# Kernel tuning notes

Hardware: AMD Instinct MI355X
Metric: run time of the kernel (lower is better)

The kernel has to match this reference:

```python
import jax, jax.numpy as jnp
import numpy as np

N_NODES = 50000
N_EDGES = 800000
IN_C = 128
OUT_C = 128


def setup_inputs() -> dict:
    key = jax.random.key(0)
    k1, k2, k3 = jax.random.split(key, 3)
    x = jax.random.normal(k1, (N_NODES, IN_C), dtype=jnp.float32)
    edge_index = jax.random.randint(k2, (2, N_EDGES), 0, N_NODES, dtype=jnp.int64)
    weight = jax.random.normal(k3, (IN_C, OUT_C), dtype=jnp.float32) * 0.01
    bias = jnp.zeros((OUT_C,), dtype=jnp.float32)
    return {"x": x, "edge_index": edge_index, "weight": weight, "bias": bias}


def reference(x, edge_index, weight, bias):
    num_nodes = x.shape[0]
    # add self-loops
    loop = jnp.arange(num_nodes, dtype=edge_index.dtype)
    src = jnp.concatenate([edge_index[0], loop])  # [E + N]
    dst = jnp.concatenate([edge_index[1], loop])  # [E + N]
    # in-degree (incl. self-loops) via scatter-add
    deg = jax.ops.segment_sum(jnp.ones_like(dst, dtype=x.dtype), dst,
                              num_segments=num_nodes)
    # deg >= 1 due to self-loops, but guard inf like the original
    deg_inv_sqrt = jnp.where(deg > 0, jax.lax.rsqrt(deg), 0.0)
    norm = deg_inv_sqrt[src] * deg_inv_sqrt[dst]  # [E + N]
    x_transformed = x @ weight  # [N, out_c]
    messages = x_transformed[src] * norm[:, None]  # [E + N, out_c]
    out = jax.ops.segment_sum(messages, dst, num_segments=num_nodes)
    return out + bias
```

## Files before the change

### kernel.cpp

```cpp
#include <hip/hip_runtime.h>

#define C 128
#define CHUNK 4096

typedef short bf16x8 __attribute__((ext_vector_type(8)));
typedef float f32x4 __attribute__((ext_vector_type(4)));

__device__ inline unsigned short f2bf(float f) {
    unsigned u = __float_as_uint(f);
    u += 0x7fffu + ((u >> 16) & 1u);
    return (unsigned short)(u >> 16);
}

__device__ inline unsigned pk2bf(float lo, float hi) {
    return (unsigned)f2bf(lo) | ((unsigned)f2bf(hi) << 16);
}

__global__ __launch_bounds__(256) void k1_hist(
        const int* __restrict__ ei, int e, int* __restrict__ H,
        int nblocks, int nbuck,
        const float* __restrict__ W, unsigned short* __restrict__ Wt) {
    int b = blockIdx.x;
    int t = threadIdx.x;
    if (b >= nblocks) {
        int i = (b - nblocks) * 256 + t;
        int nn = i >> 7, k = i & 127;
        Wt[nn * 128 + k] = f2bf(W[k * 128 + nn]);
        return;
    }
    __shared__ int h[256];
    h[t] = 0;
    __syncthreads();
    int base = b * CHUNK;
    int lim = min(CHUNK, e - base);
    for (int i = t; i < lim; i += 256)
        atomicAdd(&h[ei[e + base + i] >> 8], 1);
    __syncthreads();
    if (t < nbuck) H[t * nblocks + b] = h[t];
}

__global__ __launch_bounds__(256) void k2a_rowscan(
        int* __restrict__ H, int* __restrict__ tot, int nblocks) {
    __shared__ int s[256];
    int g = blockIdx.x, t = threadIdx.x;
    int v = (t < nblocks) ? H[g * nblocks + t] : 0;
    s[t] = v;
    __syncthreads();
    for (int off = 1; off < 256; off <<= 1) {
        int u = (t >= off) ? s[t - off] : 0;
        __syncthreads();
        s[t] += u;
        __syncthreads();
    }
    if (t < nblocks) H[g * nblocks + t] = s[t] - v;
    if (t == 255) tot[g] = s[255];
}

__global__ __launch_bounds__(256) void k2b_bucketscan(
        const int* __restrict__ tot, int* __restrict__ bbase, int nbuck, int e) {
    __shared__ int s[256];
    int t = threadIdx.x;
    int v = (t < nbuck) ? tot[t] : 0;
    s[t] = v;
    __syncthreads();
    for (int off = 1; off < 256; off <<= 1) {
        int u = (t >= off) ? s[t - off] : 0;
        __syncthreads();
        s[t] += u;
        __syncthreads();
    }
    if (t < nbuck) bbase[t] = s[t] - v;
    if (t == 0) bbase[nbuck] = e;
}

__global__ __launch_bounds__(256) void k3_scatter(
        const int* __restrict__ ei, int e, const int* __restrict__ H,
        const int* __restrict__ bbase,
        unsigned* __restrict__ staging, int nblocks, int nbuck) {
    __shared__ int cur[256];
    int b = blockIdx.x, t = threadIdx.x;
    if (t < nbuck) cur[t] = bbase[t] + H[t * nblocks + b];
    __syncthreads();
    int base = b * CHUNK;
    int lim = min(CHUNK, e - base);
    for (int i = t; i < lim; i += 256) {
        int src = ei[base + i];
        int dst = ei[e + base + i];
        int pos = atomicAdd(&cur[dst >> 8], 1);
        staging[pos] = (unsigned)src | ((unsigned)(dst & 255) << 16);
    }
}

__global__ __launch_bounds__(256) void k4_finalize(
        const unsigned* __restrict__ staging, const int* __restrict__ bbase,
        int* __restrict__ row_ptr, float* __restrict__ dis,
        unsigned short* __restrict__ srcs, int n) {
    __shared__ int sc[256];
    __shared__ int cur[256];
    int g = blockIdx.x, t = threadIdx.x;
    int s0 = bbase[g], s1 = bbase[g + 1];
    sc[t] = 0;
    __syncthreads();
    for (int i = s0 + t; i < s1; i += 256)
        atomicAdd(&sc[staging[i] >> 16], 1);
    __syncthreads();
    int v = sc[t];
    __syncthreads();
    for (int off = 1; off < 256; off <<= 1) {
        int u = (t >= off) ? sc[t - off] : 0;
        __syncthreads();
        sc[t] += u;
        __syncthreads();
    }
    int excl = sc[t] - v;
    int idx = g * 256 + t;
    if (idx <= n) row_ptr[idx] = s0 + excl;
    if (idx < n) dis[idx] = rsqrtf((float)(v + 1));
    cur[t] = s0 + excl;
    __syncthreads();
    for (int i = s0 + t; i < s1; i += 256) {
        unsigned rec = staging[i];
        int pos = atomicAdd(&cur[rec >> 16], 1);
        srcs[pos] = (unsigned short)(rec & 0xffffu);
    }
}

__global__ __launch_bounds__(256) void gemm_mfma(
        const float* __restrict__ x, const unsigned short* __restrict__ Wt,
        const float* __restrict__ dis, unsigned short* __restrict__ xts, int n) {
    const int lane = threadIdx.x & 63;
    const int wave = threadIdx.x >> 6;
    const int m = lane & 15;
    const int q = lane >> 4;
    const int r0 = blockIdx.x * 64 + wave * 16;
    const int row = r0 + m;
    const int rowc = (row < n) ? row : (n - 1);

    f32x4 acc[8];
#pragma unroll
    for (int nt = 0; nt < 8; ++nt) acc[nt] = (f32x4){0.f, 0.f, 0.f, 0.f};

#pragma unroll
    for (int kb = 0; kb < 4; ++kb) {
        const int k0 = kb * 32 + q * 8;
        const float4* xp = (const float4*)(x + (size_t)rowc * 128 + k0);
        float4 xa = xp[0];
        float4 xb = xp[1];
        union { unsigned u[4]; bf16x8 v; } af;
        af.u[0] = pk2bf(xa.x, xa.y);
        af.u[1] = pk2bf(xa.z, xa.w);
        af.u[2] = pk2bf(xb.x, xb.y);
        af.u[3] = pk2bf(xb.z, xb.w);
#pragma unroll
        for (int nt = 0; nt < 8; ++nt) {
            bf16x8 bf = *(const bf16x8*)(Wt + (size_t)(nt * 16 + m) * 128 + k0);
            acc[nt] = __builtin_amdgcn_mfma_f32_16x16x32_bf16(af.v, bf, acc[nt], 0, 0, 0);
        }
    }

    float dv[4];
    int gr[4];
#pragma unroll
    for (int r = 0; r < 4; ++r) {
        gr[r] = r0 + q * 4 + r;
        dv[r] = dis[(gr[r] < n) ? gr[r] : (n - 1)];
    }
#pragma unroll
    for (int nt = 0; nt < 8; ++nt) {
        int col = nt * 16 + m;
#pragma unroll
        for (int r = 0; r < 4; ++r) {
            if (gr[r] < n)
                xts[(size_t)gr[r] * 128 + col] = f2bf(acc[nt][r] * dv[r]);
        }
    }
}

__device__ inline void acc8(float* a, uint4 w) {
    a[0] += __uint_as_float(w.x << 16);
    a[1] += __uint_as_float(w.x & 0xffff0000u);
    a[2] += __uint_as_float(w.y << 16);
    a[3] += __uint_as_float(w.y & 0xffff0000u);
    a[4] += __uint_as_float(w.z << 16);
    a[5] += __uint_as_float(w.z & 0xffff0000u);
    a[6] += __uint_as_float(w.w << 16);
    a[7] += __uint_as_float(w.w & 0xffff0000u);
}

__global__ void gather3(const int* __restrict__ row_ptr,
                        const unsigned short* __restrict__ srcs,
                        const unsigned short* __restrict__ xts,
                        const float* __restrict__ dis,
                        const float* __restrict__ bias, float* __restrict__ out, int n) {
    int node = blockIdx.x * 16 + (threadIdx.x >> 4);
    int q = threadIdx.x & 15;
    if (node >= n) return;
    const uint4* x4 = (const uint4*)xts;
    int start = row_ptr[node];
    int end = row_ptr[node + 1];
    float a0[8] = {0, 0, 0, 0, 0, 0, 0, 0};
    float a1[8] = {0, 0, 0, 0, 0, 0, 0, 0};
    acc8(a0, x4[node * 16 + q]);
    int j = start;
    for (; j + 4 <= end; j += 4) {
        uint4 m0 = x4[(int)srcs[j] * 16 + q];
        uint4 m1 = x4[(int)srcs[j + 1] * 16 + q];
        uint4 m2 = x4[(int)srcs[j + 2] * 16 + q];
        uint4 m3 = x4[(int)srcs[j + 3] * 16 + q];
        acc8(a0, m0);
        acc8(a1, m1);
        acc8(a0, m2);
        acc8(a1, m3);
    }
    for (; j < end; ++j) acc8(a0, x4[(int)srcs[j] * 16 + q]);
    float d = dis[node];
    const float4 b0 = ((const float4*)bias)[q * 2];
    const float4 b1 = ((const float4*)bias)[q * 2 + 1];
    float4 o0, o1;
    o0.x = (a0[0] + a1[0]) * d + b0.x;
    o0.y = (a0[1] + a1[1]) * d + b0.y;
    o0.z = (a0[2] + a1[2]) * d + b0.z;
    o0.w = (a0[3] + a1[3]) * d + b0.w;
    o1.x = (a0[4] + a1[4]) * d + b1.x;
    o1.y = (a0[5] + a1[5]) * d + b1.y;
    o1.z = (a0[6] + a1[6]) * d + b1.z;
    o1.w = (a0[7] + a1[7]) * d + b1.w;
    float4* op = (float4*)(out + node * 128 + q * 8);
    op[0] = o0;
    op[1] = o1;
}

extern "C" void kernel_launch(void* const* d_in, const int* in_sizes, int n_in,
                              void* d_out, int out_size, void* d_ws, size_t ws_size,
                              hipStream_t stream) {
    const float* x    = (const float*)d_in[0];
    const int*   ei   = (const int*)d_in[1];
    const float* W    = (const float*)d_in[2];
    const float* bias = (const float*)d_in[3];
    float* out = (float*)d_out;

    const int n = in_sizes[0] / C;
    const int e = in_sizes[1] / 2;
    const int nblocks = (e + CHUNK - 1) / CHUNK;
    const int nbuck = (n + 255) >> 8;

    char* p = (char*)d_ws;
    auto alloc = [&](size_t bytes) {
        char* r = p;
        p += (bytes + 15) & ~(size_t)15;
        return (void*)r;
    };
    int*      H       = (int*)alloc((size_t)nbuck * nblocks * 4);
    int*      tot     = (int*)alloc(nbuck * 4);
    int*      bbase   = (int*)alloc((nbuck + 1) * 4);
    unsigned* staging = (unsigned*)alloc((size_t)e * 4);
    int*      row_ptr = (int*)alloc((n + 1) * 4);
    float*    dis     = (float*)alloc(n * 4);
    unsigned short* srcs = (unsigned short*)alloc((size_t)e * 2);
    unsigned short* xts  = (unsigned short*)alloc((size_t)n * C * 2);
    unsigned short* Wt   = (unsigned short*)alloc(128 * 128 * 2);

    k1_hist<<<nblocks + 64, 256, 0, stream>>>(ei, e, H, nblocks, nbuck, W, Wt);
    k2a_rowscan<<<nbuck, 256, 0, stream>>>(H, tot, nblocks);
    k2b_bucketscan<<<1, 256, 0, stream>>>(tot, bbase, nbuck, e);
    k3_scatter<<<nblocks, 256, 0, stream>>>(ei, e, H, bbase, staging, nblocks, nbuck);
    k4_finalize<<<nbuck, 256, 0, stream>>>(staging, bbase, row_ptr, dis, srcs, n);
    gemm_mfma<<<(n + 63) / 64, 256, 0, stream>>>(x, Wt, dis, xts, n);
    gather3<<<(n + 15) / 16, 256, 0, stream>>>(row_ptr, srcs, xts, dis, bias, out, n);
}
```

Measured before the change: 160.7 us.

## Overlap GEMM with CSR build stages and move source normalization into gather

The GEMM no longer scales rows by the degree factor. It is split into three slices that run as extra blocks inside the row-scan, bucket-scan and scatter kernels, so the transform overlaps the latency-bound CSR construction steps and one launch disappears. The gather now loads dis[src] for each edge and applies it with an FMA, adding a scalar gather per edge. CHUNK is halved, so the row scan loops over 256-wide segments, and k4 caches staging records in shared memory to avoid a second global read.

```diff
diff --git a/kernel.cpp b/kernel.cpp
--- a/kernel.cpp
+++ b/kernel.cpp
@@ -1,7 +1,8 @@
 #include <hip/hip_runtime.h>
 
 #define C 128
-#define CHUNK 4096
+#define CHUNK 2048
+#define K4CAP 6144
 
 typedef short bf16x8 __attribute__((ext_vector_type(8)));
 typedef float f32x4 __attribute__((ext_vector_type(4)));
@@ -14,6 +15,50 @@
 
 __device__ inline unsigned pk2bf(float lo, float hi) {
     return (unsigned)f2bf(lo) | ((unsigned)f2bf(hi) << 16);
+}
+
+__device__ inline void gemm_rows(const float* __restrict__ x,
+                                 const unsigned short* __restrict__ Wt,
+                                 unsigned short* __restrict__ xts, int n, int blk) {
+    const int t = threadIdx.x;
+    const int lane = t & 63;
+    const int wave = t >> 6;
+    const int m = lane & 15;
+    const int q = lane >> 4;
+    const int r0 = blk * 64 + wave * 16;
+    const int row = r0 + m;
+    const int rowc = (row < n) ? row : (n - 1);
+
+    f32x4 acc[8];
+#pragma unroll
+    for (int nt = 0; nt < 8; ++nt) acc[nt] = (f32x4){0.f, 0.f, 0.f, 0.f};
+
+#pragma unroll
+    for (int kb = 0; kb < 4; ++kb) {
+        const int k0 = kb * 32 + q * 8;
+        const float4* xp = (const float4*)(x + (size_t)rowc * 128 + k0);
+        float4 xa = xp[0];
+        float4 xb = xp[1];
+        union { unsigned u[4]; bf16x8 v; } af;
+        af.u[0] = pk2bf(xa.x, xa.y);
+        af.u[1] = pk2bf(xa.z, xa.w);
+        af.u[2] = pk2bf(xb.x, xb.y);
+        af.u[3] = pk2bf(xb.z, xb.w);
+#pragma unroll
+        for (int nt = 0; nt < 8; ++nt) {
+            bf16x8 bf = *(const bf16x8*)(Wt + (size_t)(nt * 16 + m) * 128 + k0);
+            acc[nt] = __builtin_amdgcn_mfma_f32_16x16x32_bf16(af.v, bf, acc[nt], 0, 0, 0);
+        }
+    }
+#pragma unroll
+    for (int nt = 0; nt < 8; ++nt) {
+        int col = nt * 16 + m;
+#pragma unroll
+        for (int r = 0; r < 4; ++r) {
+            int gr = r0 + q * 4 + r;
+            if (gr < n) xts[(size_t)gr * 128 + col] = f2bf(acc[nt][r]);
+        }
+    }
 }
 
 __global__ __launch_bounds__(256) void k1_hist(
@@ -39,11 +84,47 @@
     if (t < nbuck) H[t * nblocks + b] = h[t];
 }
 
-__global__ __launch_bounds__(256) void k2a_rowscan(
-        int* __restrict__ H, int* __restrict__ tot, int nblocks) {
+__global__ __launch_bounds__(256) void k2a_gemm(
+        int* __restrict__ H, int* __restrict__ tot, int nblocks, int nbuck,
+        const float* __restrict__ x, const unsigned short* __restrict__ Wt,
+        unsigned short* __restrict__ xts, int n, int g0) {
     __shared__ int s[256];
-    int g = blockIdx.x, t = threadIdx.x;
-    int v = (t < nblocks) ? H[g * nblocks + t] : 0;
+    int t = threadIdx.x;
+    if ((int)blockIdx.x >= nbuck) {
+        gemm_rows(x, Wt, xts, n, g0 + (int)blockIdx.x - nbuck);
+        return;
+    }
+    int g = blockIdx.x;
+    int carry = 0;
+    for (int base = 0; base < nblocks; base += 256) {
+        int v = (base + t < nblocks) ? H[g * nblocks + base + t] : 0;
+        s[t] = v;
+        __syncthreads();
+        for (int off = 1; off < 256; off <<= 1) {
+            int u = (t >= off) ? s[t - off] : 0;
+            __syncthreads();
+            s[t] += u;
+            __syncthreads();
+        }
+        if (base + t < nblocks) H[g * nblocks + base + t] = carry + s[t] - v;
+        int bs = s[255];
+        __syncthreads();
+        carry += bs;
+    }
+    if (t == 0) tot[g] = carry;
+}
+
+__global__ __launch_bounds__(256) void k2b_gemm(
+        const int* __restrict__ tot, int* __restrict__ bbase, int nbuck, int e,
+        const float* __restrict__ x, const unsigned short* __restrict__ Wt,
+        unsigned short* __restrict__ xts, int n, int g0) {
+    __shared__ int s[256];
+    int t = threadIdx.x;
+    if (blockIdx.x > 0) {
+        gemm_rows(x, Wt, xts, n, g0 + (int)blockIdx.x - 1);
+        return;
+    }
+    int v = (t < nbuck) ? tot[t] : 0;
     s[t] = v;
     __syncthreads();
     for (int off = 1; off < 256; off <<= 1) {
@@ -52,33 +133,23 @@
         s[t] += u;
         __syncthreads();
     }
-    if (t < nblocks) H[g * nblocks + t] = s[t] - v;
-    if (t == 255) tot[g] = s[255];
-}
-
-__global__ __launch_bounds__(256) void k2b_bucketscan(
-        const int* __restrict__ tot, int* __restrict__ bbase, int nbuck, int e) {
-    __shared__ int s[256];
-    int t = threadIdx.x;
-    int v = (t < nbuck) ? tot[t] : 0;
-    s[t] = v;
-    __syncthreads();
-    for (int off = 1; off < 256; off <<= 1) {
-        int u = (t >= off) ? s[t - off] : 0;
-        __syncthreads();
-        s[t] += u;
-        __syncthreads();
-    }
     if (t < nbuck) bbase[t] = s[t] - v;
     if (t == 0) bbase[nbuck] = e;
 }
 
-__global__ __launch_bounds__(256) void k3_scatter(
+__global__ __launch_bounds__(256) void k3_gemm(
         const int* __restrict__ ei, int e, const int* __restrict__ H,
-        const int* __restrict__ bbase,
-        unsigned* __restrict__ staging, int nblocks, int nbuck) {
+        const int* __restrict__ bbase, unsigned* __restrict__ staging,
+        int nblocks, int nbuck,
+        const float* __restrict__ x, const unsigned short* __restrict__ Wt,
+        unsigned short* __restrict__ xts, int n, int g0) {
     __shared__ int cur[256];
-    int b = blockIdx.x, t = threadIdx.x;
+    int t = threadIdx.x;
+    if ((int)blockIdx.x >= nblocks) {
+        gemm_rows(x, Wt, xts, n, g0 + (int)blockIdx.x - nblocks);
+        return;
+    }
+    int b = blockIdx.x;
     if (t < nbuck) cur[t] = bbase[t] + H[t * nblocks + b];
     __syncthreads();
     int base = b * CHUNK;
@@ -95,14 +166,19 @@
         const unsigned* __restrict__ staging, const int* __restrict__ bbase,
         int* __restrict__ row_ptr, float* __restrict__ dis,
         unsigned short* __restrict__ srcs, int n) {
+    __shared__ unsigned rec[K4CAP];
     __shared__ int sc[256];
     __shared__ int cur[256];
     int g = blockIdx.x, t = threadIdx.x;
     int s0 = bbase[g], s1 = bbase[g + 1];
+    int cnt = s1 - s0;
     sc[t] = 0;
     __syncthreads();
-    for (int i = s0 + t; i < s1; i += 256)
-        atomicAdd(&sc[staging[i] >> 16], 1);
+    for (int li = t; li < cnt; li += 256) {
+        unsigned r = staging[s0 + li];
+        if (li < K4CAP) rec[li] = r;
+        atomicAdd(&sc[r >> 16], 1);
+    }
     __syncthreads();
     int v = sc[t];
     __syncthreads();
@@ -118,76 +194,25 @@
     if (idx < n) dis[idx] = rsqrtf((float)(v + 1));
     cur[t] = s0 + excl;
     __syncthreads();
-    for (int i = s0 + t; i < s1; i += 256) {
-        unsigned rec = staging[i];
-        int pos = atomicAdd(&cur[rec >> 16], 1);
-        srcs[pos] = (unsigned short)(rec & 0xffffu);
-    }
-}
-
-__global__ __launch_bounds__(256) void gemm_mfma(
-        const float* __restrict__ x, const unsigned short* __restrict__ Wt,
-        const float* __restrict__ dis, unsigned short* __restrict__ xts, int n) {
-    const int lane = threadIdx.x & 63;
-    const int wave = threadIdx.x >> 6;
-    const int m = lane & 15;
-    const int q = lane >> 4;
-    const int r0 = blockIdx.x * 64 + wave * 16;
-    const int row = r0 + m;
-    const int rowc = (row < n) ? row : (n - 1);
-
-    f32x4 acc[8];
-#pragma unroll
-    for (int nt = 0; nt < 8; ++nt) acc[nt] = (f32x4){0.f, 0.f, 0.f, 0.f};
-
-#pragma unroll
-    for (int kb = 0; kb < 4; ++kb) {
-        const int k0 = kb * 32 + q * 8;
-        const float4* xp = (const float4*)(x + (size_t)rowc * 128 + k0);
-        float4 xa = xp[0];
-        float4 xb = xp[1];
-        union { unsigned u[4]; bf16x8 v; } af;
-        af.u[0] = pk2bf(xa.x, xa.y);
-        af.u[1] = pk2bf(xa.z, xa.w);
-        af.u[2] = pk2bf(xb.x, xb.y);
-        af.u[3] = pk2bf(xb.z, xb.w);
-#pragma unroll
-        for (int nt = 0; nt < 8; ++nt) {
-            bf16x8 bf = *(const bf16x8*)(Wt + (size_t)(nt * 16 + m) * 128 + k0);
-            acc[nt] = __builtin_amdgcn_mfma_f32_16x16x32_bf16(af.v, bf, acc[nt], 0, 0, 0);
-        }
-    }
-
-    float dv[4];
-    int gr[4];
-#pragma unroll
-    for (int r = 0; r < 4; ++r) {
-        gr[r] = r0 + q * 4 + r;
-        dv[r] = dis[(gr[r] < n) ? gr[r] : (n - 1)];
-    }
-#pragma unroll
-    for (int nt = 0; nt < 8; ++nt) {
-        int col = nt * 16 + m;
-#pragma unroll
-        for (int r = 0; r < 4; ++r) {
-            if (gr[r] < n)
-                xts[(size_t)gr[r] * 128 + col] = f2bf(acc[nt][r] * dv[r]);
-        }
-    }
-}
-
-__device__ inline void acc8(float* a, uint4 w) {
-    a[0] += __uint_as_float(w.x << 16);
-    a[1] += __uint_as_float(w.x & 0xffff0000u);
-    a[2] += __uint_as_float(w.y << 16);
-    a[3] += __uint_as_float(w.y & 0xffff0000u);
-    a[4] += __uint_as_float(w.z << 16);
-    a[5] += __uint_as_float(w.z & 0xffff0000u);
-    a[6] += __uint_as_float(w.w << 16);
-    a[7] += __uint_as_float(w.w & 0xffff0000u);
-}
-
-__global__ void gather3(const int* __restrict__ row_ptr,
+    for (int li = t; li < cnt; li += 256) {
+        unsigned r = (li < K4CAP) ? rec[li] : staging[s0 + li];
+        int pos = atomicAdd(&cur[r >> 16], 1);
+        srcs[pos] = (unsigned short)(r & 0xffffu);
+    }
+}
+
+__device__ inline void fma8(float* a, uint4 w, float s) {
+    a[0] = fmaf(__uint_as_float(w.x << 16), s, a[0]);
+    a[1] = fmaf(__uint_as_float(w.x & 0xffff0000u), s, a[1]);
+    a[2] = fmaf(__uint_as_float(w.y << 16), s, a[2]);
+    a[3] = fmaf(__uint_as_float(w.y & 0xffff0000u), s, a[3]);
+    a[4] = fmaf(__uint_as_float(w.z << 16), s, a[4]);
+    a[5] = fmaf(__uint_as_float(w.z & 0xffff0000u), s, a[5]);
+    a[6] = fmaf(__uint_as_float(w.w << 16), s, a[6]);
+    a[7] = fmaf(__uint_as_float(w.w & 0xffff0000u), s, a[7]);
+}
+
+__global__ void gather4(const int* __restrict__ row_ptr,
                         const unsigned short* __restrict__ srcs,
                         const unsigned short* __restrict__ xts,
                         const float* __restrict__ dis,
@@ -196,24 +221,29 @@
     int q = threadIdx.x & 15;
     if (node >= n) return;
     const uint4* x4 = (const uint4*)xts;
+    float d = dis[node];
     int start = row_ptr[node];
     int end = row_ptr[node + 1];
     float a0[8] = {0, 0, 0, 0, 0, 0, 0, 0};
     float a1[8] = {0, 0, 0, 0, 0, 0, 0, 0};
-    acc8(a0, x4[node * 16 + q]);
+    fma8(a0, x4[node * 16 + q], d);
     int j = start;
     for (; j + 4 <= end; j += 4) {
-        uint4 m0 = x4[(int)srcs[j] * 16 + q];
-        uint4 m1 = x4[(int)srcs[j + 1] * 16 + q];
-        uint4 m2 = x4[(int)srcs[j + 2] * 16 + q];
-        uint4 m3 = x4[(int)srcs[j + 3] * 16 + q];
-        acc8(a0, m0);
-        acc8(a1, m1);
-        acc8(a0, m2);
-        acc8(a1, m3);
-    }
-    for (; j < end; ++j) acc8(a0, x4[(int)srcs[j] * 16 + q]);
-    float d = dis[node];
+        int s0 = srcs[j], s1 = srcs[j + 1], s2 = srcs[j + 2], s3 = srcs[j + 3];
+        float w0 = dis[s0], w1 = dis[s1], w2 = dis[s2], w3 = dis[s3];
+        uint4 m0 = x4[s0 * 16 + q];
+        uint4 m1 = x4[s1 * 16 + q];
+        uint4 m2 = x4[s2 * 16 + q];
+        uint4 m3 = x4[s3 * 16 + q];
+        fma8(a0, m0, w0);
+        fma8(a1, m1, w1);
+        fma8(a0, m2, w2);
+        fma8(a1, m3, w3);
+    }
+    for (; j < end; ++j) {
+        int s = srcs[j];
+        fma8(a0, x4[s * 16 + q], dis[s]);
+    }
     const float4 b0 = ((const float4*)bias)[q * 2];
     const float4 b1 = ((const float4*)bias)[q * 2 + 1];
     float4 o0, o1;
@@ -243,6 +273,11 @@
     const int e = in_sizes[1] / 2;
     const int nblocks = (e + CHUNK - 1) / CHUNK;
     const int nbuck = (n + 255) >> 8;
+
+    const int G = (n + 63) / 64;
+    const int gA = G / 3;
+    const int gB = G / 3;
+    const int gC = G - gA - gB;
 
     char* p = (char*)d_ws;
     auto alloc = [&](size_t bytes) {
@@ -261,10 +296,13 @@
     unsigned short* Wt   = (unsigned short*)alloc(128 * 128 * 2);
 
     k1_hist<<<nblocks + 64, 256, 0, stream>>>(ei, e, H, nblocks, nbuck, W, Wt);
-    k2a_rowscan<<<nbuck, 256, 0, stream>>>(H, tot, nblocks);
-    k2b_bucketscan<<<1, 256, 0, stream>>>(tot, bbase, nbuck, e);
-    k3_scatter<<<nblocks, 256, 0, stream>>>(ei, e, H, bbase, staging, nblocks, nbuck);
+    k2a_gemm<<<nbuck + gA, 256, 0, stream>>>(H, tot, nblocks, nbuck,
+                                             x, Wt, xts, n, 0);
+    k2b_gemm<<<1 + gB, 256, 0, stream>>>(tot, bbase, nbuck, e,
+                                         x, Wt, xts, n, gA);
+    k3_gemm<<<nblocks + gC, 256, 0, stream>>>(ei, e, H, bbase, staging,
+                                              nblocks, nbuck,
+                                              x, Wt, xts, n, gA + gB);
     k4_finalize<<<nbuck, 256, 0, stream>>>(staging, bbase, row_ptr, dis, srcs, n);
-    gemm_mfma<<<(n + 63) / 64, 256, 0, stream>>>(x, Wt, dis, xts, n);
-    gather3<<<(n + 15) / 16, 256, 0, stream>>>(row_ptr, srcs, xts, dis, bias, out, n);
-}
+    gather4<<<(n + 15) / 16, 256, 0, stream>>>(row_ptr, srcs, xts, dis, bias, out, n);
+}
```

New measurement: 168.7 us. 1.05x slower.
